# Kernel optimization log

Hardware: AMD Instinct MI355X
Metric: run time of the kernel (lower is better)

Reference implementation:

```python
import jax, jax.numpy as jnp
import numpy as np
import math

H = 16
D_MODEL = 1024
D_K = D_MODEL // H


def setup_inputs() -> dict:
    key = jax.random.key(0)
    ks = jax.random.split(key, 11)
    B, S = 2, 2048
    scale = 1.0 / math.sqrt(D_MODEL)
    inp = {
        "query": jax.random.normal(ks[0], (B, S, D_MODEL), dtype=jnp.float32),
        "key": jax.random.normal(ks[1], (B, S, D_MODEL), dtype=jnp.float32),
        "value": jax.random.normal(ks[2], (B, S, D_MODEL), dtype=jnp.float32),
        # torch nn.Linear convention: W is [out_features, in_features]
        "Wq": jax.random.normal(ks[3], (D_MODEL, D_MODEL), dtype=jnp.float32) * scale,
        "bq": jnp.zeros((D_MODEL,), dtype=jnp.float32),
        "Wk": jax.random.normal(ks[4], (D_MODEL, D_MODEL), dtype=jnp.float32) * scale,
        "bk": jnp.zeros((D_MODEL,), dtype=jnp.float32),
        "Wv": jax.random.normal(ks[5], (D_MODEL, D_MODEL), dtype=jnp.float32) * scale,
        "bv": jnp.zeros((D_MODEL,), dtype=jnp.float32),
        "Wo": jax.random.normal(ks[6], (D_MODEL, D_MODEL), dtype=jnp.float32) * scale,
        "bo": jnp.zeros((D_MODEL,), dtype=jnp.float32),
    }
    return inp


def _split_heads(x):
    # [b, s, h*d_k] -> [b, h, s, d_k]
    b, s, _ = x.shape
    return x.reshape(b, s, H, D_K).transpose(0, 2, 1, 3)


def reference(query, key, value, Wq, bq, Wk, bk, Wv, bv, Wo, bo):
    q = _split_heads(query @ Wq.T + bq)
    k = _split_heads(key @ Wk.T + bk)
    v = _split_heads(value @ Wv.T + bv)
    # scaled dot-product attention, full L x L scores per head
    scores = jnp.einsum("bhqd,bhkd->bhqk", q, k) / math.sqrt(D_K)
    attn = jax.nn.softmax(scores, axis=-1)
    ctx = jnp.einsum("bhqk,bhkd->bhqd", attn, v)  # [b, h, s, d_k]
    b, h, s, d = ctx.shape
    ctx = ctx.transpose(0, 2, 1, 3).reshape(b, s, h * d)
    return ctx @ Wo.T + bo
```

## Files before the change

kernel.cpp:

```cpp
#include <hip/hip_runtime.h>

typedef unsigned int u32;
typedef unsigned short u16;
typedef __attribute__((ext_vector_type(8))) short short8;
typedef __attribute__((ext_vector_type(4))) float f32x4;
typedef __attribute__((ext_vector_type(2))) u32 u32x2;
typedef __attribute__((ext_vector_type(4))) u32 u32x4;

#define DEV __device__ __forceinline__

DEV u16 f2bf(float f) {
  u32 u = __builtin_bit_cast(u32, f);
  u = (u + 0x7FFFu + ((u >> 16) & 1u)) >> 16;
  return (u16)u;
}

DEV float fexp2(float x) {
#if __has_builtin(__builtin_amdgcn_exp2f)
  return __builtin_amdgcn_exp2f(x);
#else
  return exp2f(x);
#endif
}

DEV u32 cvt_pk_bf16(float lo, float hi) {
  u32 r;
  asm("v_cvt_pk_bf16_f32 %0, %1, %2" : "=v"(r) : "v"(lo), "v"(hi));
  return r;
}

DEV void llds16(const void* g, void* lds) {
  __builtin_amdgcn_global_load_lds(
      (const __attribute__((address_space(1))) u32*)g,
      (__attribute__((address_space(3))) u32*)lds, 16, 0, 0);
}

struct CvtArgs {
  const float* src[7];
  u16* dst[7];
};

__global__ void cvt_all(CvtArgs ca) {
  int i = blockIdx.x * blockDim.x + threadIdx.x;
  int chunk = i >> 17;
  int seg = chunk < 12 ? (chunk >> 2) : (chunk - 9);
  u32 base8 = (seg < 3) ? (u32)seg * 524288u : 1572864u + ((u32)seg - 3) * 131072u;
  size_t off = ((size_t)i - base8) * 8;
  const f32x4* p = (const f32x4*)(ca.src[seg] + off);
  f32x4 a = p[0], b = p[1];
  short8 o;
  o[0] = (short)f2bf(a[0]); o[1] = (short)f2bf(a[1]);
  o[2] = (short)f2bf(a[2]); o[3] = (short)f2bf(a[3]);
  o[4] = (short)f2bf(b[0]); o[5] = (short)f2bf(b[1]);
  o[6] = (short)f2bf(b[2]); o[7] = (short)f2bf(b[3]);
  *(short8*)(ca.dst[seg] + off) = o;
}

struct GemmArgs {
  const u16* A[3];
  const u16* W[3];
  const float* bias[3];
  void* C[3];
  float scale[3];
};

template <int BM, int BN, int WAVES_M, int OUT_BF16>
__global__ __launch_bounds__(256, 2) void gemm_bt(GemmArgs ga) {
  constexpr int K = 1024, N = 1024;
  constexpr int WAVES_N = 4 / WAVES_M;
  constexpr int WM = BM / WAVES_M, WN = BN / WAVES_N;
  constexpr int AM = WM / 16, AN = WN / 16;
  constexpr int SEGS = (BM + BN) / 16;
  constexpr int PW = SEGS / 4;

  __shared__ u16 lsA[BM * 32];
  __shared__ u16 lsB[BN * 32];

  const int z = blockIdx.z;
  const u16* __restrict__ A = ga.A[z];
  const u16* __restrict__ W = ga.W[z];
  const int tid = threadIdx.x;
  const int l = tid & 63, w = tid >> 6;
  const int lg = l >> 4, lr = l & 15;
  const int bn = blockIdx.x, bm = blockIdx.y;
  const int wm = w / WAVES_N, wn = w % WAVES_N;

  f32x4 acc[AM][AN];
#pragma unroll
  for (int i = 0; i < AM; ++i)
#pragma unroll
    for (int j = 0; j < AN; ++j) acc[i][j] = (f32x4){0.f, 0.f, 0.f, 0.f};

  for (int k0 = 0; k0 < K; k0 += 32) {
    __syncthreads();
#pragma unroll
    for (int i = 0; i < PW; ++i) {
      int s = w * PW + i;
      if (s < BM / 16) {
        u32 sb = s * 1024;
        u32 lb = sb + l * 16;
        u32 row = lb >> 6, colS = (lb & 63) >> 1;
        llds16(A + (size_t)(bm * BM + row) * K + k0 + colS, (char*)lsA + sb);
      } else {
        u32 sb = (u32)(s - BM / 16) * 1024;
        u32 lb = sb + l * 16;
        u32 row = lb >> 6, colS = (lb & 63) >> 1;
        llds16(W + (size_t)(bn * BN + row) * K + k0 + colS, (char*)lsB + sb);
      }
    }
    __syncthreads();
    short8 af[AM], bf[AN];
#pragma unroll
    for (int i = 0; i < AM; ++i)
      af[i] = *(const short8*)&lsA[(wm * WM + i * 16 + lr) * 32 + lg * 8];
#pragma unroll
    for (int j = 0; j < AN; ++j)
      bf[j] = *(const short8*)&lsB[(wn * WN + j * 16 + lr) * 32 + lg * 8];
#pragma unroll
    for (int i = 0; i < AM; ++i)
#pragma unroll
      for (int j = 0; j < AN; ++j)
        acc[i][j] = __builtin_amdgcn_mfma_f32_16x16x32_bf16(af[i], bf[j], acc[i][j], 0, 0, 0);
  }

  const float sc = ga.scale[z];
  const float* __restrict__ bias = ga.bias[z];
#pragma unroll
  for (int j = 0; j < AN; ++j) {
    int col = bn * BN + wn * WN + j * 16 + lr;
    float bv = bias[col];
#pragma unroll
    for (int i = 0; i < AM; ++i) {
      int row0 = bm * BM + wm * WM + i * 16 + lg * 4;
#pragma unroll
      for (int r = 0; r < 4; ++r) {
        float v = (acc[i][j][r] + bv) * sc;
        if constexpr (OUT_BF16)
          ((u16*)ga.C[z])[(size_t)(row0 + r) * N + col] = f2bf(v);
        else
          ((float*)ga.C[z])[(size_t)(row0 + r) * N + col] = v;
      }
    }
  }
}

__global__ __launch_bounds__(256, 2) void attn_fwd(
    const u16* __restrict__ Q, const u16* __restrict__ Kp,
    const u16* __restrict__ V, u16* __restrict__ O) {
  constexpr int S = 2048, LD = 1024;
  __shared__ u16 Kt[2][64 * 64];
  __shared__ u16 Vt[2][64 * 64];
  const int tid = threadIdx.x;
  const int l = tid & 63, w = tid >> 6;
  const int lg = l >> 4, lr = l & 15;
  const int qt = blockIdx.x, h = blockIdx.y, b = blockIdx.z;
  const size_t base = ((size_t)b * S) * LD + h * 64;
  const int q0 = qt * 128 + w * 32;

  short8 qf[2][2];
#pragma unroll
  for (int g = 0; g < 2; ++g)
#pragma unroll
    for (int c = 0; c < 2; ++c)
      qf[g][c] = *(const short8*)&Q[base + (size_t)(q0 + g * 16 + lr) * LD + c * 32 + lg * 8];

  f32x4 acc[2][4];
#pragma unroll
  for (int g = 0; g < 2; ++g)
#pragma unroll
    for (int i = 0; i < 4; ++i) acc[g][i] = (f32x4){0.f, 0.f, 0.f, 0.f};
  float lsum[2] = {0.f, 0.f};

  const int m = tid & 31;
  const int kp0 = m * 2;
  const int key0 = ((m & 16) << 1) + ((m & 2) << 3) + (((m >> 2) & 3) << 2) + ((m & 1) << 1);
  const int vd0 = (tid >> 5) * 8;

#define KSTAGE(T, BUF)                                                          \
  {                                                                             \
    _Pragma("unroll") for (int i_ = 0; i_ < 2; ++i_) {                          \
      u32 sb = (u32)(w * 2 + i_) * 1024;                                        \
      u32 lb = sb + l * 16;                                                     \
      u32 key = lb >> 7;                                                        \
      u32 inner = (lb & 127) ^ ((key & 7) << 4);                                \
      llds16(Kp + base + (size_t)((T) * 64 + key) * LD + (inner >> 1),          \
             (char*)Kt[BUF] + sb);                                              \
    }                                                                           \
  }
#define VWRITE(BUF, VA, VB)                                                     \
  {                                                                             \
    _Pragma("unroll") for (int jj = 0; jj < 8; ++jj) {                          \
      u32 pv = (u32)(u16)(VA)[jj] | ((u32)(u16)(VB)[jj] << 16);                 \
      u32 addr = (u32)((vd0 + jj) * 128 + kp0 * 2) ^ ((u32)jj << 4);            \
      *(u32*)((char*)Vt[BUF] + addr) = pv;                                      \
    }                                                                           \
  }

  {
    short8 va = *(const short8*)&V[base + (size_t)key0 * LD + vd0];
    short8 vb = *(const short8*)&V[base + (size_t)(key0 + 1) * LD + vd0];
    KSTAGE(0, 0);
    VWRITE(0, va, vb);
  }
  __syncthreads();

  int cur = 0;
  for (int t = 0; t < 32; ++t) {
    const int kb = t * 64;
    short8 nva, nvb;
    if (t < 31) {
      nva = *(const short8*)&V[base + (size_t)(kb + 64 + key0) * LD + vd0];
      nvb = *(const short8*)&V[base + (size_t)(kb + 64 + key0 + 1) * LD + vd0];
      KSTAGE(t + 1, cur ^ 1);
    }

    f32x4 sv[2][4];
    __builtin_amdgcn_s_setprio(1);
#pragma unroll
    for (int ks = 0; ks < 4; ++ks) {
      u32 a0 = (u32)(((ks * 16 + lr) * 128 + lg * 16) ^ ((lr & 7) << 4));
      short8 kf0 = *(const short8*)((const char*)Kt[cur] + a0);
      short8 kf1 = *(const short8*)((const char*)Kt[cur] + (a0 ^ 64));
#pragma unroll
      for (int g = 0; g < 2; ++g) {
        f32x4 s = (f32x4){0.f, 0.f, 0.f, 0.f};
        s = __builtin_amdgcn_mfma_f32_16x16x32_bf16(kf0, qf[g][0], s, 0, 0, 0);
        s = __builtin_amdgcn_mfma_f32_16x16x32_bf16(kf1, qf[g][1], s, 0, 0, 0);
        sv[g][ks] = s;
      }
    }
    __builtin_amdgcn_s_setprio(0);

    u32 pk[2][8];
#pragma unroll
    for (int g = 0; g < 2; ++g) {
#pragma unroll
      for (int ks = 0; ks < 4; ++ks) {
#pragma unroll
        for (int r = 0; r < 4; ++r) {
          float e = fexp2(sv[g][ks][r]);
          sv[g][ks][r] = e;
          lsum[g] += e;
        }
        pk[g][ks * 2 + 0] = cvt_pk_bf16(sv[g][ks][0], sv[g][ks][1]);
        pk[g][ks * 2 + 1] = cvt_pk_bf16(sv[g][ks][2], sv[g][ks][3]);
      }
    }

    __builtin_amdgcn_s_setprio(1);
#pragma unroll
    for (int ds = 0; ds < 4; ++ds) {
#pragma unroll
      for (int c = 0; c < 2; ++c) {
        u32 va_ = (u32)(((ds * 16 + lr) * 128 + c * 64 + lg * 16) ^ ((lr & 7) << 4));
        short8 vf = *(const short8*)((const char*)Vt[cur] + va_);
#pragma unroll
        for (int g = 0; g < 2; ++g) {
          u32x4 pc = {pk[g][c * 4 + 0], pk[g][c * 4 + 1], pk[g][c * 4 + 2], pk[g][c * 4 + 3]};
          short8 pf = __builtin_bit_cast(short8, pc);
          acc[g][ds] = __builtin_amdgcn_mfma_f32_16x16x32_bf16(vf, pf, acc[g][ds], 0, 0, 0);
        }
      }
    }
    __builtin_amdgcn_s_setprio(0);

    if (t < 31) VWRITE(cur ^ 1, nva, nvb);
    __syncthreads();
    cur ^= 1;
  }

#pragma unroll
  for (int g = 0; g < 2; ++g) {
    lsum[g] += __shfl_xor(lsum[g], 16);
    lsum[g] += __shfl_xor(lsum[g], 32);
  }
#pragma unroll
  for (int g = 0; g < 2; ++g) {
    float inv = __builtin_amdgcn_rcpf(lsum[g]);
#pragma unroll
    for (int ds = 0; ds < 4; ++ds) {
      u32x2 ov;
      ov[0] = cvt_pk_bf16(acc[g][ds][0] * inv, acc[g][ds][1] * inv);
      ov[1] = cvt_pk_bf16(acc[g][ds][2] * inv, acc[g][ds][3] * inv);
      *(u32x2*)&O[base + (size_t)(q0 + g * 16 + lr) * LD + ds * 16 + lg * 4] = ov;
    }
  }
#undef KSTAGE
#undef VWRITE
}

extern "C" void kernel_launch(void* const* d_in, const int* in_sizes, int n_in,
                              void* d_out, int out_size, void* d_ws, size_t ws_size,
                              hipStream_t stream) {
  constexpr size_t SZ_X = 4096ull * 1024;
  constexpr size_t SZ_W = 1024ull * 1024;
  const float* bq = (const float*)d_in[4];
  const float* bk = (const float*)d_in[6];
  const float* bv = (const float*)d_in[8];
  const float* bo = (const float*)d_in[10];

  char* ws = (char*)d_ws;
  u16* xq = (u16*)ws;
  u16* xk = xq + SZ_X;
  u16* xv = xk + SZ_X;
  u16* wqb = xv + SZ_X;
  u16* wkb = wqb + SZ_W;
  u16* wvb = wkb + SZ_W;
  u16* wob = wvb + SZ_W;
  u16* Qp = wob + SZ_W;
  u16* Kp = Qp + SZ_X;
  u16* Vp = Kp + SZ_X;
  u16* Cx = Vp + SZ_X;

  CvtArgs ca;
  ca.src[0] = (const float*)d_in[0]; ca.dst[0] = xq;
  ca.src[1] = (const float*)d_in[1]; ca.dst[1] = xk;
  ca.src[2] = (const float*)d_in[2]; ca.dst[2] = xv;
  ca.src[3] = (const float*)d_in[3]; ca.dst[3] = wqb;
  ca.src[4] = (const float*)d_in[5]; ca.dst[4] = wkb;
  ca.src[5] = (const float*)d_in[7]; ca.dst[5] = wvb;
  ca.src[6] = (const float*)d_in[9]; ca.dst[6] = wob;
  cvt_all<<<dim3(8192), 256, 0, stream>>>(ca);

  GemmArgs g1;
  g1.A[0] = xq;  g1.A[1] = xk;  g1.A[2] = xv;
  g1.W[0] = wqb; g1.W[1] = wkb; g1.W[2] = wvb;
  g1.bias[0] = bq; g1.bias[1] = bk; g1.bias[2] = bv;
  g1.C[0] = Qp; g1.C[1] = Kp; g1.C[2] = Vp;
  g1.scale[0] = 0.18033688011112042f;
  g1.scale[1] = 1.f; g1.scale[2] = 1.f;
  gemm_bt<128, 128, 2, 1><<<dim3(8, 32, 3), 256, 0, stream>>>(g1);

  attn_fwd<<<dim3(16, 16, 2), 256, 0, stream>>>(Qp, Kp, Vp, Cx);

  GemmArgs g2 = {};
  g2.A[0] = Cx; g2.W[0] = wob; g2.bias[0] = bo; g2.C[0] = d_out; g2.scale[0] = 1.f;
  gemm_bt<64, 128, 1, 0><<<dim3(8, 64, 1), 256, 0, stream>>>(g2);
}
```

Measured before the change: 140.2 us.

## Split attention over the key dimension in two halves with a combine kernel

The attention kernel now splits the 32 key tiles into two halves across blockIdx.z, doubling the grid to 1024 blocks and raising the launch-bounds occupancy hint. Each half writes unnormalized fp32 accumulators and row sums, and a new combine kernel adds them, normalizes and converts to bf16. The goal is better CU utilization for the original 512-block grid. The cost is extra fp32 global traffic (about 32MB written and read) plus an extra launch. The workspace reuse and borrowing d_out as scratch depend on ordering with the projection inputs, and there is no running max, so this relies on the inputs keeping scores bounded, as the code before already did.

```diff
diff --git a/kernel.cpp b/kernel.cpp
--- a/kernel.cpp
+++ b/kernel.cpp
@@ -144,16 +144,20 @@
   }
 }
 
-__global__ __launch_bounds__(256, 2) void attn_fwd(
+__global__ __launch_bounds__(256, 4) void attn_fwd(
     const u16* __restrict__ Q, const u16* __restrict__ Kp,
-    const u16* __restrict__ V, u16* __restrict__ O) {
+    const u16* __restrict__ V, float* __restrict__ acc0,
+    float* __restrict__ acc1, float* __restrict__ lsOut) {
   constexpr int S = 2048, LD = 1024;
   __shared__ u16 Kt[2][64 * 64];
   __shared__ u16 Vt[2][64 * 64];
   const int tid = threadIdx.x;
   const int l = tid & 63, w = tid >> 6;
   const int lg = l >> 4, lr = l & 15;
-  const int qt = blockIdx.x, h = blockIdx.y, b = blockIdx.z;
+  const int qt = blockIdx.x, h = blockIdx.y;
+  const int b = blockIdx.z >> 1, half = blockIdx.z & 1;
+  const int t0 = half * 16;
+  float* __restrict__ aOut = half ? acc1 : acc0;
   const size_t base = ((size_t)b * S) * LD + h * 64;
   const int q0 = qt * 128 + w * 32;
 
@@ -197,21 +201,21 @@
   }
 
   {
-    short8 va = *(const short8*)&V[base + (size_t)key0 * LD + vd0];
-    short8 vb = *(const short8*)&V[base + (size_t)(key0 + 1) * LD + vd0];
-    KSTAGE(0, 0);
+    short8 va = *(const short8*)&V[base + (size_t)(t0 * 64 + key0) * LD + vd0];
+    short8 vb = *(const short8*)&V[base + (size_t)(t0 * 64 + key0 + 1) * LD + vd0];
+    KSTAGE(t0, 0);
     VWRITE(0, va, vb);
   }
   __syncthreads();
 
   int cur = 0;
-  for (int t = 0; t < 32; ++t) {
-    const int kb = t * 64;
+  for (int t = 0; t < 16; ++t) {
+    const int kb = (t0 + t) * 64;
     short8 nva, nvb;
-    if (t < 31) {
+    if (t < 15) {
       nva = *(const short8*)&V[base + (size_t)(kb + 64 + key0) * LD + vd0];
       nvb = *(const short8*)&V[base + (size_t)(kb + 64 + key0 + 1) * LD + vd0];
-      KSTAGE(t + 1, cur ^ 1);
+      KSTAGE(t0 + t + 1, cur ^ 1);
     }
 
     f32x4 sv[2][4];
@@ -236,14 +240,11 @@
     for (int g = 0; g < 2; ++g) {
 #pragma unroll
       for (int ks = 0; ks < 4; ++ks) {
-#pragma unroll
-        for (int r = 0; r < 4; ++r) {
-          float e = fexp2(sv[g][ks][r]);
-          sv[g][ks][r] = e;
-          lsum[g] += e;
-        }
-        pk[g][ks * 2 + 0] = cvt_pk_bf16(sv[g][ks][0], sv[g][ks][1]);
-        pk[g][ks * 2 + 1] = cvt_pk_bf16(sv[g][ks][2], sv[g][ks][3]);
+        float e0 = fexp2(sv[g][ks][0]), e1 = fexp2(sv[g][ks][1]);
+        float e2 = fexp2(sv[g][ks][2]), e3 = fexp2(sv[g][ks][3]);
+        lsum[g] += (e0 + e1) + (e2 + e3);
+        pk[g][ks * 2 + 0] = cvt_pk_bf16(e0, e1);
+        pk[g][ks * 2 + 1] = cvt_pk_bf16(e2, e3);
       }
     }
 
@@ -264,7 +265,7 @@
     }
     __builtin_amdgcn_s_setprio(0);
 
-    if (t < 31) VWRITE(cur ^ 1, nva, nvb);
+    if (t < 15) VWRITE(cur ^ 1, nva, nvb);
     __syncthreads();
     cur ^= 1;
   }
@@ -276,17 +277,34 @@
   }
 #pragma unroll
   for (int g = 0; g < 2; ++g) {
-    float inv = __builtin_amdgcn_rcpf(lsum[g]);
-#pragma unroll
-    for (int ds = 0; ds < 4; ++ds) {
-      u32x2 ov;
-      ov[0] = cvt_pk_bf16(acc[g][ds][0] * inv, acc[g][ds][1] * inv);
-      ov[1] = cvt_pk_bf16(acc[g][ds][2] * inv, acc[g][ds][3] * inv);
-      *(u32x2*)&O[base + (size_t)(q0 + g * 16 + lr) * LD + ds * 16 + lg * 4] = ov;
-    }
+    size_t rb = base + (size_t)(q0 + g * 16 + lr) * LD;
+#pragma unroll
+    for (int ds = 0; ds < 4; ++ds)
+      *(f32x4*)&aOut[rb + ds * 16 + lg * 4] = acc[g][ds];
+    if (lg == 0)
+      lsOut[(size_t)half * 65536 + ((size_t)b * S + q0 + g * 16 + lr) * 16 + h] = lsum[g];
   }
 #undef KSTAGE
 #undef VWRITE
+}
+
+__global__ void attn_combine(const float* __restrict__ a0, const float* __restrict__ a1,
+                             const float* __restrict__ ls, u16* __restrict__ out) {
+  int i = blockIdx.x * blockDim.x + threadIdx.x;
+  int row = i >> 7;
+  int rem = i & 127;
+  int h = rem >> 3;
+  size_t off = (size_t)row * 1024 + rem * 8;
+  f32x4 x0 = *(const f32x4*)&a0[off], x1 = *(const f32x4*)&a0[off + 4];
+  f32x4 y0 = *(const f32x4*)&a1[off], y1 = *(const f32x4*)&a1[off + 4];
+  float lv = ls[(size_t)row * 16 + h] + ls[65536 + (size_t)row * 16 + h];
+  float inv = __builtin_amdgcn_rcpf(lv);
+  u32x4 o;
+  o[0] = cvt_pk_bf16((x0[0] + y0[0]) * inv, (x0[1] + y0[1]) * inv);
+  o[1] = cvt_pk_bf16((x0[2] + y0[2]) * inv, (x0[3] + y0[3]) * inv);
+  o[2] = cvt_pk_bf16((x1[0] + y1[0]) * inv, (x1[1] + y1[1]) * inv);
+  o[3] = cvt_pk_bf16((x1[2] + y1[2]) * inv, (x1[3] + y1[3]) * inv);
+  *(u32x4*)&out[off] = o;
 }
 
 extern "C" void kernel_launch(void* const* d_in, const int* in_sizes, int n_in,
@@ -312,6 +330,10 @@
   u16* Vp = Kp + SZ_X;
   u16* Cx = Vp + SZ_X;
 
+  float* acc0 = (float*)ws;
+  float* accLs = (float*)(ws + 16 * 1024 * 1024);
+  float* acc1 = (float*)d_out;
+
   CvtArgs ca;
   ca.src[0] = (const float*)d_in[0]; ca.dst[0] = xq;
   ca.src[1] = (const float*)d_in[1]; ca.dst[1] = xk;
@@ -331,7 +353,8 @@
   g1.scale[1] = 1.f; g1.scale[2] = 1.f;
   gemm_bt<128, 128, 2, 1><<<dim3(8, 32, 3), 256, 0, stream>>>(g1);
 
-  attn_fwd<<<dim3(16, 16, 2), 256, 0, stream>>>(Qp, Kp, Vp, Cx);
+  attn_fwd<<<dim3(16, 16, 4), 256, 0, stream>>>(Qp, Kp, Vp, acc0, acc1, accLs);
+  attn_combine<<<dim3(2048), 256, 0, stream>>>(acc0, acc1, accLs, Cx);
 
   GemmArgs g2 = {};
   g2.A[0] = Cx; g2.W[0] = wob; g2.bias[0] = bo; g2.C[0] = d_out; g2.scale[0] = 1.f;
```

New measurement: 143.6 us. 1.02x slower.

## Fuse fp32-to-bf16 activation conversion into QKV projection GEMM tile loads

Applied to the files above, without the earlier changes.

The separate conversion kernel no longer converts the three fp32 activation tensors. It now converts only the four weight matrices, also using packed bf16 conversion instructions. The QKV GEMM instead reads fp32 activations directly, converts them in registers, and writes bf16 into LDS, so the bf16 activation copies are never written to or read back from global memory. The trade-off is that A-tile loads become synchronous register loads instead of async global-to-LDS loads, which may expose more latency. The attention exp loop is also restructured slightly with a tree sum.

```diff
diff --git a/kernel.cpp b/kernel.cpp
--- a/kernel.cpp
+++ b/kernel.cpp
@@ -35,49 +35,44 @@
       (__attribute__((address_space(3))) u32*)lds, 16, 0, 0);
 }
 
-struct CvtArgs {
-  const float* src[7];
-  u16* dst[7];
+struct CvtW {
+  const float* src[4];
+  u16* dst[4];
 };
 
-__global__ void cvt_all(CvtArgs ca) {
+__global__ void cvt_w(CvtW cw) {
   int i = blockIdx.x * blockDim.x + threadIdx.x;
-  int chunk = i >> 17;
-  int seg = chunk < 12 ? (chunk >> 2) : (chunk - 9);
-  u32 base8 = (seg < 3) ? (u32)seg * 524288u : 1572864u + ((u32)seg - 3) * 131072u;
-  size_t off = ((size_t)i - base8) * 8;
-  const f32x4* p = (const f32x4*)(ca.src[seg] + off);
+  int seg = i >> 17;
+  size_t off = ((size_t)(i & 131071)) * 8;
+  const f32x4* p = (const f32x4*)(cw.src[seg] + off);
   f32x4 a = p[0], b = p[1];
-  short8 o;
-  o[0] = (short)f2bf(a[0]); o[1] = (short)f2bf(a[1]);
-  o[2] = (short)f2bf(a[2]); o[3] = (short)f2bf(a[3]);
-  o[4] = (short)f2bf(b[0]); o[5] = (short)f2bf(b[1]);
-  o[6] = (short)f2bf(b[2]); o[7] = (short)f2bf(b[3]);
-  *(short8*)(ca.dst[seg] + off) = o;
+  u32x4 o;
+  o[0] = cvt_pk_bf16(a[0], a[1]);
+  o[1] = cvt_pk_bf16(a[2], a[3]);
+  o[2] = cvt_pk_bf16(b[0], b[1]);
+  o[3] = cvt_pk_bf16(b[2], b[3]);
+  *(u32x4*)(cw.dst[seg] + off) = o;
 }
 
 struct GemmArgs {
-  const u16* A[3];
+  const void* A[3];
   const u16* W[3];
   const float* bias[3];
   void* C[3];
   float scale[3];
 };
 
-template <int BM, int BN, int WAVES_M, int OUT_BF16>
+template <int BM, int BN, int WAVES_M, int OUT_BF16, int A_F32>
 __global__ __launch_bounds__(256, 2) void gemm_bt(GemmArgs ga) {
   constexpr int K = 1024, N = 1024;
   constexpr int WAVES_N = 4 / WAVES_M;
   constexpr int WM = BM / WAVES_M, WN = BN / WAVES_N;
   constexpr int AM = WM / 16, AN = WN / 16;
-  constexpr int SEGS = (BM + BN) / 16;
-  constexpr int PW = SEGS / 4;
 
   __shared__ u16 lsA[BM * 32];
   __shared__ u16 lsB[BN * 32];
 
   const int z = blockIdx.z;
-  const u16* __restrict__ A = ga.A[z];
   const u16* __restrict__ W = ga.W[z];
   const int tid = threadIdx.x;
   const int l = tid & 63, w = tid >> 6;
@@ -93,19 +88,47 @@
 
   for (int k0 = 0; k0 < K; k0 += 32) {
     __syncthreads();
-#pragma unroll
-    for (int i = 0; i < PW; ++i) {
-      int s = w * PW + i;
-      if (s < BM / 16) {
-        u32 sb = s * 1024;
-        u32 lb = sb + l * 16;
-        u32 row = lb >> 6, colS = (lb & 63) >> 1;
-        llds16(A + (size_t)(bm * BM + row) * K + k0 + colS, (char*)lsA + sb);
-      } else {
-        u32 sb = (u32)(s - BM / 16) * 1024;
+    if constexpr (A_F32) {
+      const float* __restrict__ Af = (const float*)ga.A[z];
+#pragma unroll
+      for (int i = 0; i < BN / 64; ++i) {
+        u32 sb = (u32)(w * (BN / 64) + i) * 1024;
         u32 lb = sb + l * 16;
         u32 row = lb >> 6, colS = (lb & 63) >> 1;
         llds16(W + (size_t)(bn * BN + row) * K + k0 + colS, (char*)lsB + sb);
+      }
+      {
+        constexpr int TPR = 256 / BM;
+        int row = tid / TPR, kh = tid % TPR;
+        const f32x4* src = (const f32x4*)(Af + (size_t)(bm * BM + row) * K + k0 + kh * 16);
+        f32x4 f0 = src[0], f1 = src[1], f2 = src[2], f3 = src[3];
+        u32x4 o0, o1;
+        o0[0] = cvt_pk_bf16(f0[0], f0[1]); o0[1] = cvt_pk_bf16(f0[2], f0[3]);
+        o0[2] = cvt_pk_bf16(f1[0], f1[1]); o0[3] = cvt_pk_bf16(f1[2], f1[3]);
+        o1[0] = cvt_pk_bf16(f2[0], f2[1]); o1[1] = cvt_pk_bf16(f2[2], f2[3]);
+        o1[2] = cvt_pk_bf16(f3[0], f3[1]); o1[3] = cvt_pk_bf16(f3[2], f3[3]);
+        char* dst = (char*)lsA + row * 64 + kh * 32;
+        *(u32x4*)dst = o0;
+        *(u32x4*)(dst + 16) = o1;
+      }
+    } else {
+      const u16* __restrict__ A = (const u16*)ga.A[z];
+      constexpr int SEGS = (BM + BN) / 16;
+      constexpr int PW = SEGS / 4;
+#pragma unroll
+      for (int i = 0; i < PW; ++i) {
+        int s = w * PW + i;
+        if (s < BM / 16) {
+          u32 sb = s * 1024;
+          u32 lb = sb + l * 16;
+          u32 row = lb >> 6, colS = (lb & 63) >> 1;
+          llds16(A + (size_t)(bm * BM + row) * K + k0 + colS, (char*)lsA + sb);
+        } else {
+          u32 sb = (u32)(s - BM / 16) * 1024;
+          u32 lb = sb + l * 16;
+          u32 row = lb >> 6, colS = (lb & 63) >> 1;
+          llds16(W + (size_t)(bn * BN + row) * K + k0 + colS, (char*)lsB + sb);
+        }
       }
     }
     __syncthreads();
@@ -236,14 +259,11 @@
     for (int g = 0; g < 2; ++g) {
 #pragma unroll
       for (int ks = 0; ks < 4; ++ks) {
-#pragma unroll
-        for (int r = 0; r < 4; ++r) {
-          float e = fexp2(sv[g][ks][r]);
-          sv[g][ks][r] = e;
-          lsum[g] += e;
-        }
-        pk[g][ks * 2 + 0] = cvt_pk_bf16(sv[g][ks][0], sv[g][ks][1]);
-        pk[g][ks * 2 + 1] = cvt_pk_bf16(sv[g][ks][2], sv[g][ks][3]);
+        float e0 = fexp2(sv[g][ks][0]), e1 = fexp2(sv[g][ks][1]);
+        float e2 = fexp2(sv[g][ks][2]), e3 = fexp2(sv[g][ks][3]);
+        lsum[g] += (e0 + e1) + (e2 + e3);
+        pk[g][ks * 2 + 0] = cvt_pk_bf16(e0, e1);
+        pk[g][ks * 2 + 1] = cvt_pk_bf16(e2, e3);
       }
     }
 
@@ -300,10 +320,7 @@
   const float* bo = (const float*)d_in[10];
 
   char* ws = (char*)d_ws;
-  u16* xq = (u16*)ws;
-  u16* xk = xq + SZ_X;
-  u16* xv = xk + SZ_X;
-  u16* wqb = xv + SZ_X;
+  u16* wqb = (u16*)ws;
   u16* wkb = wqb + SZ_W;
   u16* wvb = wkb + SZ_W;
   u16* wob = wvb + SZ_W;
@@ -312,28 +329,25 @@
   u16* Vp = Kp + SZ_X;
   u16* Cx = Vp + SZ_X;
 
-  CvtArgs ca;
-  ca.src[0] = (const float*)d_in[0]; ca.dst[0] = xq;
-  ca.src[1] = (const float*)d_in[1]; ca.dst[1] = xk;
-  ca.src[2] = (const float*)d_in[2]; ca.dst[2] = xv;
-  ca.src[3] = (const float*)d_in[3]; ca.dst[3] = wqb;
-  ca.src[4] = (const float*)d_in[5]; ca.dst[4] = wkb;
-  ca.src[5] = (const float*)d_in[7]; ca.dst[5] = wvb;
-  ca.src[6] = (const float*)d_in[9]; ca.dst[6] = wob;
-  cvt_all<<<dim3(8192), 256, 0, stream>>>(ca);
+  CvtW cw;
+  cw.src[0] = (const float*)d_in[3]; cw.dst[0] = wqb;
+  cw.src[1] = (const float*)d_in[5]; cw.dst[1] = wkb;
+  cw.src[2] = (const float*)d_in[7]; cw.dst[2] = wvb;
+  cw.src[3] = (const float*)d_in[9]; cw.dst[3] = wob;
+  cvt_w<<<dim3(2048), 256, 0, stream>>>(cw);
 
   GemmArgs g1;
-  g1.A[0] = xq;  g1.A[1] = xk;  g1.A[2] = xv;
+  g1.A[0] = d_in[0]; g1.A[1] = d_in[1]; g1.A[2] = d_in[2];
   g1.W[0] = wqb; g1.W[1] = wkb; g1.W[2] = wvb;
   g1.bias[0] = bq; g1.bias[1] = bk; g1.bias[2] = bv;
   g1.C[0] = Qp; g1.C[1] = Kp; g1.C[2] = Vp;
   g1.scale[0] = 0.18033688011112042f;
   g1.scale[1] = 1.f; g1.scale[2] = 1.f;
-  gemm_bt<128, 128, 2, 1><<<dim3(8, 32, 3), 256, 0, stream>>>(g1);
+  gemm_bt<128, 128, 2, 1, 1><<<dim3(8, 32, 3), 256, 0, stream>>>(g1);
 
   attn_fwd<<<dim3(16, 16, 2), 256, 0, stream>>>(Qp, Kp, Vp, Cx);
 
   GemmArgs g2 = {};
   g2.A[0] = Cx; g2.W[0] = wob; g2.bias[0] = bo; g2.C[0] = d_out; g2.scale[0] = 1.f;
-  gemm_bt<64, 128, 1, 0><<<dim3(8, 64, 1), 256, 0, stream>>>(g2);
-}
+  gemm_bt<64, 128, 1, 0, 0><<<dim3(8, 64, 1), 256, 0, stream>>>(g2);
+}
```

Result: slower. 153.4 us (+9.4%).
